# Optimization experiments

Measured on AMD Instinct MI355X. Metric: run time of the kernel, lower is better.

The kernel has to match this reference:

```python
import jax, jax.numpy as jnp
import numpy as np

B, N = 8, 200          # images, padded detections per image
IMG = 640.0            # nominal image size for box coordinates
ALLOWED_CLASSES = (1, 2, 3, 5, 7)  # roi_model.allowed_class_idxs
SCORE_THR = 0.001


def _make_boxes(key, b, n):
    k1, k2, k3, k4 = jax.random.split(key, 4)
    cxy = jax.random.uniform(k1, (b, n, 2), minval=0.0, maxval=IMG)
    wh = jax.random.uniform(k2, (b, n, 2), minval=10.0, maxval=120.0)
    xy1 = cxy - wh / 2.0
    xy2 = cxy + wh / 2.0
    score = jax.random.uniform(k3, (b, n, 1))
    cls = jax.random.randint(k4, (b, n, 1), 0, 10).astype(jnp.float32)
    return jnp.concatenate([xy1, xy2, score, cls], axis=-1)  # [b,n,6]


def setup_inputs() -> dict:
    key = jax.random.key(0)
    k1, k2 = jax.random.split(key)
    return {"boxes1": _make_boxes(k1, B, N), "boxes2": _make_boxes(k2, B, N)}


def _valid(boxes):
    cls = boxes[..., 5].astype(jnp.int32)
    allowed = jnp.zeros(cls.shape, dtype=bool)
    for c in ALLOWED_CLASSES:
        allowed = allowed | (cls == c)
    return (boxes[..., 4] > SCORE_THR) & allowed


def _iou_matrix(b1, b2):
    """Vectorized pairwise IoU; zero where classes differ or a box is filtered out."""
    v1, v2 = _valid(b1), _valid(b2)
    x1 = jnp.maximum(b1[:, :, None, 0], b2[:, None, :, 0])
    y1 = jnp.maximum(b1[:, :, None, 1], b2[:, None, :, 1])
    x2 = jnp.minimum(b1[:, :, None, 2], b2[:, None, :, 2])
    y2 = jnp.minimum(b1[:, :, None, 3], b2[:, None, :, 3])
    inter = jnp.maximum(x2 - x1, 0.0) * jnp.maximum(y2 - y1, 0.0)  # [B,N,N]
    a1 = (b1[..., 2] - b1[..., 0]) * (b1[..., 3] - b1[..., 1])
    a2 = (b2[..., 2] - b2[..., 0]) * (b2[..., 3] - b2[..., 1])
    union = a1[:, :, None] + a2[:, None, :] - inter
    same_cls = b1[..., 5].astype(jnp.int32)[:, :, None] == b2[..., 5].astype(jnp.int32)[:, None, :]
    mask = same_cls & v1[:, :, None] & v2[:, None, :]
    return jnp.where(mask, inter / union, 0.0), v1, v2


def _hungarian(cost):
    """Exact linear sum assignment (minimize) for a square cost matrix.
    Jonker-Volgenant style shortest augmenting path, O(n^3), vectorized inner step.
    Returns col_of_row[i] = column assigned to row i. Padding rows/cols of zeros
    make this equivalent to scipy's rectangular max-IoU matching."""
    n = cost.shape[0]
    INF = np.inf
    a = np.zeros((n + 1, n + 1), dtype=np.float64)
    a[1:, 1:] = cost
    u = np.zeros(n + 1); v = np.zeros(n + 1)
    p = np.zeros(n + 1, dtype=np.int64)   # p[j] = row matched to column j (1-based)
    way = np.zeros(n + 1, dtype=np.int64)
    for i in range(1, n + 1):
        p[0] = i
        j0 = 0
        minv = np.full(n + 1, INF)
        used = np.zeros(n + 1, dtype=bool)
        while True:
            used[j0] = True
            i0 = p[j0]
            cur = a[i0] - u[i0] - v
            cand = (~used) & (cur < minv)
            minv[cand] = cur[cand]
            way[cand] = j0
            masked = np.where(used, INF, minv)
            j0 = int(masked.argmin())
            delta = masked[j0]
            u[p[used]] += delta
            v[used] -= delta
            minv[~used] -= delta
            if p[j0] == 0:
                break
        while j0 != 0:
            j1 = way[j0]
            p[j0] = p[j1]
            j0 = j1
    col_of_row = np.empty(n, dtype=np.int64)
    col_of_row[p[1:] - 1] = np.arange(n)
    return col_of_row


def _loss(iou, perm, na, nb):
    matched = jnp.take_along_axis(iou, perm[:, :, None], axis=2)[..., 0]  # [B,N]
    sum_ious = matched.sum(-1)
    # n_instances = n_pairs + leftovers on each side = max(na, nb)
    denom = jnp.maximum(jnp.maximum(na, nb), 1.0)
    per_img = 1.0 - sum_ious / denom
    both_zero = (na == 0) & (nb == 0)
    one_zero = (na == 0) != (nb == 0)
    per_img = jnp.where(both_zero, 0.0, jnp.where(one_zero, 1.0, per_img))
    return per_img.mean()


def reference(boxes1, boxes2):
    iou, v1, v2 = _iou_matrix(boxes1, boxes2)
    cost = -np.asarray(iou, dtype=np.float64)
    perm = jnp.asarray(np.stack([_hungarian(cost[b]) for b in range(cost.shape[0])]))
    na = v1.sum(-1).astype(jnp.float32)
    nb = v2.sum(-1).astype(jnp.float32)
    return _loss(iou, perm, na, nb)
```

## Files before the change

### kernel.cpp

```cpp
#include <hip/hip_runtime.h>
#include <math.h>


constexpr int BIMG = 8;
constexpr int NBOX = 200;
constexpr int NCLS = 5;
constexpr int NBLK = BIMG * NCLS;
constexpr float SCORE_THR = 0.001f;

__device__ __forceinline__ unsigned fkey(float f) {
    unsigned u = __float_as_uint(f);
    return (u & 0x80000000u) ? ~u : (u | 0x80000000u);
}
__device__ __forceinline__ float fkey_inv(unsigned k) {
    unsigned u = (k & 0x80000000u) ? (k ^ 0x80000000u) : ~k;
    return __uint_as_float(u);
}

#define ARGMIN_DPP_STEP(CTRL)                                                \
    {                                                                        \
        unsigned ok = (unsigned)__builtin_amdgcn_update_dpp(                 \
            (int)ik, (int)ik, (CTRL), 0xF, 0xF, false);                      \
        unsigned op = (unsigned)__builtin_amdgcn_update_dpp(                 \
            (int)ip, (int)ip, (CTRL), 0xF, 0xF, false);                      \
        bool lt = (ok < ik) || ((ok == ik) && (op < ip));                    \
        ik = lt ? ok : ik;                                                   \
        ip = lt ? op : ip;                                                   \
    }

__global__ void __launch_bounds__(64)
det_fused_kernel(const float* __restrict__ boxes1,
                 const float* __restrict__ boxes2,
                 float* __restrict__ sum_part,
                 int* __restrict__ m1_part, int* __restrict__ m2_part,
                 int* __restrict__ flags,
                 float* __restrict__ out)
{
    const int lane = threadIdx.x;
    const int blk  = blockIdx.x;
    const int b    = blk / NCLS;
    const int ci   = blk % NCLS;
    const int cls  = (ci == 0) ? 1 : (ci == 1) ? 2 : (ci == 2) ? 3 : (ci == 3) ? 5 : 7;

    __shared__ float r1x1[NBOX], r1y1[NBOX], r1x2[NBOX], r1y2[NBOX], r1a[NBOX];
    __shared__ float r2x1[NBOX], r2y1[NBOX], r2x2[NBOX], r2y2[NBOX], r2a[NBOX];
    __shared__ float uarr[NBOX + 1], varr[NBOX + 1], minvarr[NBOX + 1];
    __shared__ int   wayarr[NBOX + 1], parr[NBOX + 1], usedarr[NBOX + 1];

    const float* g1 = boxes1 + (size_t)b * NBOX * 6;
    const float* g2 = boxes2 + (size_t)b * NBOX * 6;
    const unsigned long long ltmask = (1ull << lane) - 1ull;

    int m1 = 0, m2 = 0;
    for (int c0 = 0; c0 < NBOX; c0 += 64) {
        int t = c0 + lane;
        bool in = (t < NBOX);
        float x1 = 0, y1 = 0, x2 = 0, y2 = 0, sc = 0, cf = 0;
        if (in) {
            const float2* p = (const float2*)(g1 + (size_t)t * 6);
            float2 q0 = p[0], q1 = p[1], q2 = p[2];
            x1 = q0.x; y1 = q0.y; x2 = q1.x; y2 = q1.y; sc = q2.x; cf = q2.y;
        }
        bool pr = in && (sc > SCORE_THR) && ((int)cf == cls);
        unsigned long long mk = __ballot(pr);
        int pos = m1 + __popcll(mk & ltmask);
        if (pr) { r1x1[pos] = x1; r1y1[pos] = y1; r1x2[pos] = x2; r1y2[pos] = y2;
                  r1a[pos] = (x2 - x1) * (y2 - y1); }
        m1 += __popcll(mk);

        if (in) {
            const float2* p = (const float2*)(g2 + (size_t)t * 6);
            float2 q0 = p[0], q1 = p[1], q2 = p[2];
            x1 = q0.x; y1 = q0.y; x2 = q1.x; y2 = q1.y; sc = q2.x; cf = q2.y;
        }
        pr = in && (sc > SCORE_THR) && ((int)cf == cls);
        mk = __ballot(pr);
        pos = m2 + __popcll(mk & ltmask);
        if (pr) { r2x1[pos] = x1; r2y1[pos] = y1; r2x2[pos] = x2; r2y2[pos] = y2;
                  r2a[pos] = (x2 - x1) * (y2 - y1); }
        m2 += __popcll(mk);
    }
    __syncthreads();

    float blockContrib = 0.f;

    do {
        if (m1 == 0 || m2 == 0) break;
        const int n = (m1 > m2) ? m1 : m2;

        if (n <= 64) {
            const bool swapped = (m1 > m2);
            float* rrx1 = swapped ? r2x1 : r1x1; float* rry1 = swapped ? r2y1 : r1y1;
            float* rrx2 = swapped ? r2x2 : r1x2; float* rry2 = swapped ? r2y2 : r1y2;
            float* rra  = swapped ? r2a  : r1a;
            float* ccx1 = swapped ? r1x1 : r2x1; float* ccy1 = swapped ? r1y1 : r2y1;
            float* ccx2 = swapped ? r1x2 : r2x2; float* ccy2 = swapped ? r1y2 : r2y2;
            float* cca  = swapped ? r1a  : r2a;
            int mr = swapped ? m2 : m1;
            int mc = swapped ? m1 : m2;

            float rbx1 = 0, rby1 = 0, rbx2 = 0, rby2 = 0, rba = 0;
            if (lane < mr) { rbx1 = rrx1[lane]; rby1 = rry1[lane]; rbx2 = rrx2[lane];
                             rby2 = rry2[lane]; rba = rra[lane]; }
            float cbx1 = 0, cby1 = 0, cbx2 = 0, cby2 = 0, cba = 0;
            if (lane < mc) { cbx1 = ccx1[lane]; cby1 = ccy1[lane]; cbx2 = ccx2[lane];
                             cby2 = ccy2[lane]; cba = cca[lane]; }

            unsigned long long rowmask = 0ull;
            bool colnz = false;
            for (int i = 0; i < mr; ++i) {
                float ax1 = rrx1[i], ay1 = rry1[i], ax2 = rrx2[i], ay2 = rry2[i];
                float iw = fminf(ax2, cbx2) - fmaxf(ax1, cbx1);
                float ih = fminf(ay2, cby2) - fmaxf(ay1, cby1);
                bool nz = (lane < mc) && (iw > 0.f) && (ih > 0.f);
                unsigned long long bal = __ballot(nz);
                if (bal) rowmask |= (1ull << i);
                colnz |= nz;
            }
            int mrP = __popcll(rowmask);
            if (mrP == 0) break;
            unsigned long long colmask = __ballot(colnz);
            int mcP = __popcll(colmask);

            __syncthreads();
            if (lane < mr && ((rowmask >> lane) & 1ull)) {
                int pos = __popcll(rowmask & ltmask);
                rrx1[pos] = rbx1; rry1[pos] = rby1; rrx2[pos] = rbx2; rry2[pos] = rby2;
                rra[pos] = rba;
            }
            if (lane < mc && ((colmask >> lane) & 1ull)) {
                int pos = __popcll(colmask & ltmask);
                ccx1[pos] = cbx1; ccy1[pos] = cby1; ccx2[pos] = cbx2; ccy2[pos] = cby2;
                cca[pos] = cba;
            }
            __syncthreads();
            rbx1 = rby1 = rbx2 = rby2 = rba = 0.f;
            if (lane < mrP) { rbx1 = rrx1[lane]; rby1 = rry1[lane]; rbx2 = rrx2[lane];
                              rby2 = rry2[lane]; rba = rra[lane]; }
            cbx1 = cby1 = cbx2 = cby2 = cba = 0.f;
            if (lane < mcP) { cbx1 = ccx1[lane]; cby1 = ccy1[lane]; cbx2 = ccx2[lane];
                              cby2 = ccy2[lane]; cba = cca[lane]; }
            if (mrP > mcP) {
                float t;
                t = rbx1; rbx1 = cbx1; cbx1 = t;  t = rby1; rby1 = cby1; cby1 = t;
                t = rbx2; rbx2 = cbx2; cbx2 = t;  t = rby2; rby2 = cby2; cby2 = t;
                t = rba;  rba  = cba;  cba  = t;
                int ti = mrP; mrP = mcP; mcP = ti;
            }

            float cmin = INFINITY; int cargmin = 0;
            for (int i = 0; i < mrP; ++i) {
                float rx1 = __shfl(rbx1, i), ry1 = __shfl(rby1, i);
                float rx2 = __shfl(rbx2, i), ry2 = __shfl(rby2, i);
                float ra  = __shfl(rba,  i);
                float iw = fmaxf(fminf(rx2, cbx2) - fmaxf(rx1, cbx1), 0.f);
                float ih = fmaxf(fminf(ry2, cby2) - fmaxf(ry1, cby1), 0.f);
                float inter = iw * ih;
                float c = (lane < mcP) ? (-(inter / (ra + cba - inter))) : 0.f;
                if (c < cmin) { cmin = c; cargmin = i; }
            }

            unsigned long long rowfree = (mrP >= 64) ? ~0ull : ((1ull << mrP) - 1ull);
            unsigned long long amask = 0ull;
            for (int j = 0; j < mcP; ++j) {
                int i = __builtin_amdgcn_readlane(cargmin, j);
                if ((rowfree >> i) & 1ull) { rowfree &= ~(1ull << i); amask |= (1ull << j); }
            }

            float vj = (lane < mcP) ? cmin : 0.f;
            float urow = 0.f;
            int   pmrow = 0;
            float cmx1 = 0, cmy1 = 0, cmx2 = 0, cmy2 = 0, cma = 0;
            {
                bool gm = (lane < mcP) && ((amask >> lane) & 1ull);
                float gx1 = __shfl(rbx1, cargmin), gy1 = __shfl(rby1, cargmin);
                float gx2 = __shfl(rbx2, cargmin), gy2 = __shfl(rby2, cargmin);
                float gar = __shfl(rba,  cargmin);
                if (gm) { pmrow = cargmin + 1;
                          cmx1 = gx1; cmy1 = gy1; cmx2 = gx2; cmy2 = gy2; cma = gar; }
            }

            for (int i = 1; i <= mrP; ++i) {
                if (!((rowfree >> (i - 1)) & 1ull)) continue;

                float rootx1 = __shfl(rbx1, i - 1), rooty1 = __shfl(rby1, i - 1);
                float rootx2 = __shfl(rbx2, i - 1), rooty2 = __shfl(rby2, i - 1);
                float roota  = __shfl(rba,  i - 1);
                float rx1 = rootx1, ry1 = rooty1, rx2 = rootx2, ry2 = rooty2, ra = roota;
                float u0 = 0.f, u_free = 0.f, minvj = INFINITY;
                int   wayj = 0, j0cur = 0, j0n = 0;
                bool  usedj = (lane >= mcP);
                bool  found = false;

                for (int guard = 0; guard <= 66; ++guard) {
                    float iou = 0.f;
                    if (lane < mcP) {
                        float iw = fmaxf(fminf(rx2, cbx2) - fmaxf(rx1, cbx1), 0.f);
                        float ih = fmaxf(fminf(ry2, cby2) - fmaxf(ry1, cby1), 0.f);
                        float inter = iw * ih;
                        iou = inter / (ra + cba - inter);
                    }
                    float cur = -iou - u0 - vj;
                    if (!usedj && cur < minvj) { minvj = cur; wayj = j0cur; }

                    unsigned ik = usedj ? 0xFFFFFFFFu : fkey(minvj);
                    unsigned ip = usedj ? 0xFFFFFFFFu
                                        : ((pmrow ? 0x100u : 0u) | (unsigned)(lane + 1));
                    ARGMIN_DPP_STEP(0xB1)
                    ARGMIN_DPP_STEP(0x4E)
                    ARGMIN_DPP_STEP(0x141)
                    ARGMIN_DPP_STEP(0x140)
                    ARGMIN_DPP_STEP(0x142)
                    ARGMIN_DPP_STEP(0x143)
                    unsigned sk = (unsigned)__builtin_amdgcn_readlane((int)ik, 63);
                    unsigned sp = (unsigned)__builtin_amdgcn_readlane((int)ip, 63);
                    float delta = fkey_inv(sk);
                    j0n = (int)(sp & 0xFFu);
                    bool j0matched = (sp & 0x100u) != 0u;
                    if (j0n == 0xFF) break;

                    u_free += delta;
                    if (usedj) { vj -= delta; if (pmrow) urow += delta; }
                    else       { minvj -= delta; }

                    if (!j0matched) { found = true; break; }

                    if (lane == j0n - 1) usedj = true;
                    u0  = __shfl(urow, j0n - 1);
                    rx1 = __shfl(cmx1, j0n - 1); ry1 = __shfl(cmy1, j0n - 1);
                    rx2 = __shfl(cmx2, j0n - 1); ry2 = __shfl(cmy2, j0n - 1);
                    ra  = __shfl(cma,  j0n - 1);
                    j0cur = j0n;
                }

                if (found) {
                    int jj = j0n;
                    for (int hop = 0; hop < 66 && jj != 0; ++hop) {
                        int j1 = __shfl(wayj, jj - 1);
                        if (j1 == 0) {
                            if (lane == jj - 1) {
                                pmrow = i; urow = u_free;
                                cmx1 = rootx1; cmy1 = rooty1; cmx2 = rootx2;
                                cmy2 = rooty2; cma = roota;
                            }
                            jj = 0;
                        } else {
                            int   ppj = __shfl(pmrow, j1 - 1);
                            float pur = __shfl(urow,  j1 - 1);
                            float px1 = __shfl(cmx1, j1 - 1), py1 = __shfl(cmy1, j1 - 1);
                            float px2 = __shfl(cmx2, j1 - 1), py2 = __shfl(cmy2, j1 - 1);
                            float pa  = __shfl(cma,  j1 - 1);
                            if (lane == jj - 1) {
                                pmrow = ppj; urow = pur;
                                cmx1 = px1; cmy1 = py1; cmx2 = px2; cmy2 = py2; cma = pa;
                            }
                            jj = j1;
                        }
                    }
                }
            }

            float contrib = 0.f;
            if (lane < mcP && pmrow != 0) {
                float iw = fmaxf(fminf(cmx2, cbx2) - fmaxf(cmx1, cbx1), 0.f);
                float ih = fmaxf(fminf(cmy2, cby2) - fmaxf(cmy1, cby1), 0.f);
                float inter = iw * ih;
                contrib = inter / (cma + cba - inter);
            }
            #pragma unroll
            for (int off = 32; off; off >>= 1) contrib += __shfl_xor(contrib, off);
            blockContrib = contrib;
        } else {
            for (int j = lane; j <= n; j += 64) { varr[j] = 0.f; parr[j] = 0; uarr[j] = 0.f; }
            __syncthreads();

            int j0 = 0;
            for (int i = 1; i <= n; ++i) {
                if (lane == 0) parr[0] = i;
                for (int j = lane; j <= n; j += 64) { minvarr[j] = INFINITY; usedarr[j] = 0; }
                j0 = 0;
                __syncthreads();

                for (int it = 0; it <= n + 1; ++it) {
                    if (lane == 0) usedarr[j0] = 1;
                    __syncthreads();
                    const int i0 = parr[j0];
                    const float u0 = uarr[i0];
                    const bool rowReal = (i0 <= m1);
                    float rx1 = 0, ry1 = 0, rx2 = 0, ry2 = 0, ra = 0;
                    if (rowReal) { rx1 = r1x1[i0-1]; ry1 = r1y1[i0-1]; rx2 = r1x2[i0-1];
                                   ry2 = r1y2[i0-1]; ra = r1a[i0-1]; }
                    for (int j = lane; j <= n; j += 64) {
                        if (j >= 1 && !usedarr[j]) {
                            float cost = 0.f;
                            if (rowReal && j <= m2) {
                                float ix1 = fmaxf(rx1, r2x1[j-1]), iy1 = fmaxf(ry1, r2y1[j-1]);
                                float ix2 = fminf(rx2, r2x2[j-1]), iy2 = fminf(ry2, r2y2[j-1]);
                                float iw = fmaxf(ix2 - ix1, 0.f), ih = fmaxf(iy2 - iy1, 0.f);
                                float inter = iw * ih;
                                cost = -(inter / (ra + r2a[j-1] - inter));
                            }
                            float cur = cost - u0 - varr[j];
                            if (cur < minvarr[j]) { minvarr[j] = cur; wayarr[j] = j0; }
                        }
                    }
                    __syncthreads();

                    float bv = INFINITY; int bu = 0, bj = n + 1;
                    for (int j = lane; j <= n; j += 64) {
                        float m = usedarr[j] ? INFINITY : minvarr[j];
                        int   un = (parr[j] == 0) ? 1 : 0;
                        if (m < bv || (m == bv && (un > bu || (un == bu && j < bj))))
                            { bv = m; bu = un; bj = j; }
                    }
                    #pragma unroll
                    for (int off = 32; off; off >>= 1) {
                        float ov = __shfl_xor(bv, off);
                        int   ou = __shfl_xor(bu, off);
                        int   oj = __shfl_xor(bj, off);
                        if (ov < bv || (ov == bv && (ou > bu || (ou == bu && oj < bj))))
                            { bv = ov; bu = ou; bj = oj; }
                    }
                    j0 = bj;
                    const float delta = bv;
                    for (int j = lane; j <= n; j += 64) {
                        if (usedarr[j]) { uarr[parr[j]] += delta; varr[j] -= delta; }
                        else            { minvarr[j] -= delta; }
                    }
                    __syncthreads();
                    if (parr[j0] == 0) break;
                }

                if (lane == 0) {
                    int jj = j0, guard = 0;
                    while (jj != 0 && guard++ <= n + 1) {
                        int j1 = wayarr[jj];
                        parr[jj] = parr[j1];
                        jj = j1;
                    }
                }
                __syncthreads();
            }

            float contrib = 0.f;
            for (int j = lane; j <= n; j += 64) {
                if (j >= 1 && j <= m2) {
                    int pi = parr[j];
                    if (pi >= 1 && pi <= m1) {
                        float ix1 = fmaxf(r1x1[pi-1], r2x1[j-1]), iy1 = fmaxf(r1y1[pi-1], r2y1[j-1]);
                        float ix2 = fminf(r1x2[pi-1], r2x2[j-1]), iy2 = fminf(r1y2[pi-1], r2y2[j-1]);
                        float iw = fmaxf(ix2 - ix1, 0.f), ih = fmaxf(iy2 - iy1, 0.f);
                        float inter = iw * ih;
                        contrib += inter / (r1a[pi-1] + r2a[j-1] - inter);
                    }
                }
            }
            #pragma unroll
            for (int off = 32; off; off >>= 1) contrib += __shfl_xor(contrib, off);
            blockContrib = contrib;
        }
    } while (0);

    if (lane == 0) {
        sum_part[blk] = blockContrib;
        m1_part[blk]  = m1;
        m2_part[blk]  = m2;
    }
    if (blk != 0) {
        if (lane == 0)
            __hip_atomic_store(&flags[blk], 1, __ATOMIC_RELEASE, __HIP_MEMORY_SCOPE_AGENT);
        return;
    }

    if (lane >= 1 && lane < NBLK) {
        while (__hip_atomic_load(&flags[lane], __ATOMIC_ACQUIRE,
                                 __HIP_MEMORY_SCOPE_AGENT) != 1)
            __builtin_amdgcn_s_sleep(1);
    }
    float s = 0.f; int a1 = 0, a2 = 0;
    if (lane < NBLK) { s = sum_part[lane]; a1 = m1_part[lane]; a2 = m2_part[lane]; }
    float st = s; int t1 = a1, t2 = a2;
    #pragma unroll
    for (int k = 1; k < NCLS; ++k) {
        st += __shfl(s, lane + k);
        t1 += __shfl(a1, lane + k);
        t2 += __shfl(a2, lane + k);
    }
    float per;
    {
        float denom = fmaxf(fmaxf((float)t1, (float)t2), 1.f);
        float pv = 1.f - st / denom;
        bool bz = (t1 == 0) && (t2 == 0);
        bool oz = ((t1 == 0) != (t2 == 0));
        per = bz ? 0.f : (oz ? 1.f : pv);
    }
    float acc = 0.f;
    #pragma unroll
    for (int bb = 0; bb < BIMG; ++bb) acc += __shfl(per, bb * NCLS);
    if (lane == 0) out[0] = acc / (float)BIMG;
}

extern "C" void kernel_launch(void* const* d_in, const int* in_sizes, int n_in,
                              void* d_out, int out_size, void* d_ws, size_t ws_size,
                              hipStream_t stream) {
    const float* b1 = (const float*)d_in[0];
    const float* b2 = (const float*)d_in[1];
    float* sum_part = (float*)d_ws;
    int*   m1_part  = (int*)(sum_part + NBLK);
    int*   m2_part  = m1_part + NBLK;
    int*   flags    = m2_part + NBLK;

    det_fused_kernel<<<NBLK, 64, 0, stream>>>(b1, b2, sum_part, m1_part, m2_part,
                                              flags, (float*)d_out);
}
```

Baseline: 78.28 us.

## Rewrite wave-level Hungarian with float4 box layout and packed argmin keys

Box storage changes from separate per-coordinate shared arrays to float4 records, with all global loads issued up front into registers. The small-case path fuses the overlap scan with the greedy column-min computation and uses a single packed 32-bit key (truncated value plus matched flag plus lane) for the DPP argmin instead of two keys. Shuffles become readlane, and the final reduction uses DPP. Areas are recomputed instead of stored, and truncating the key's low mantissa bits can change tie-breaking and assignment results.

```diff
diff --git a/kernel.cpp b/kernel.cpp
--- a/kernel.cpp
+++ b/kernel.cpp
@@ -8,24 +8,20 @@
 constexpr int NBLK = BIMG * NCLS;
 constexpr float SCORE_THR = 0.001f;
 
-__device__ __forceinline__ unsigned fkey(float f) {
-    unsigned u = __float_as_uint(f);
-    return (u & 0x80000000u) ? ~u : (u | 0x80000000u);
-}
-__device__ __forceinline__ float fkey_inv(unsigned k) {
-    unsigned u = (k & 0x80000000u) ? (k ^ 0x80000000u) : ~k;
-    return __uint_as_float(u);
-}
-
-#define ARGMIN_DPP_STEP(CTRL)                                                \
+__device__ __forceinline__ int   rl_i(int x, int l)   { return __builtin_amdgcn_readlane(x, l); }
+__device__ __forceinline__ float rl_f(float x, int l) { return __int_as_float(__builtin_amdgcn_readlane(__float_as_int(x), l)); }
+
+#define MIN_DPP_STEP(CTRL)                                                   \
     {                                                                        \
         unsigned ok = (unsigned)__builtin_amdgcn_update_dpp(                 \
-            (int)ik, (int)ik, (CTRL), 0xF, 0xF, false);                      \
-        unsigned op = (unsigned)__builtin_amdgcn_update_dpp(                 \
-            (int)ip, (int)ip, (CTRL), 0xF, 0xF, false);                      \
-        bool lt = (ok < ik) || ((ok == ik) && (op < ip));                    \
-        ik = lt ? ok : ik;                                                   \
-        ip = lt ? op : ip;                                                   \
+            (int)key, (int)key, (CTRL), 0xF, 0xF, false);                    \
+        key = (ok < key) ? ok : key;                                         \
+    }
+#define SUM_DPP_STEP(CTRL)                                                   \
+    {                                                                        \
+        float o = __int_as_float(__builtin_amdgcn_update_dpp(                \
+            __float_as_int(acc), __float_as_int(acc), (CTRL), 0xF, 0xF, false)); \
+        acc += o;                                                            \
     }
 
 __global__ void __launch_bounds__(64)
@@ -41,44 +37,45 @@
     const int b    = blk / NCLS;
     const int ci   = blk % NCLS;
     const int cls  = (ci == 0) ? 1 : (ci == 1) ? 2 : (ci == 2) ? 3 : (ci == 3) ? 5 : 7;
-
-    __shared__ float r1x1[NBOX], r1y1[NBOX], r1x2[NBOX], r1y2[NBOX], r1a[NBOX];
-    __shared__ float r2x1[NBOX], r2y1[NBOX], r2x2[NBOX], r2y2[NBOX], r2a[NBOX];
+    const unsigned long long ltm = (1ull << lane) - 1ull;
+
+    __shared__ float4 bs1[NBOX], bs2[NBOX];
+    __shared__ float4 rcomp[64], ccomp[64];
+    __shared__ float2 cmeta[64];
     __shared__ float uarr[NBOX + 1], varr[NBOX + 1], minvarr[NBOX + 1];
     __shared__ int   wayarr[NBOX + 1], parr[NBOX + 1], usedarr[NBOX + 1];
 
     const float* g1 = boxes1 + (size_t)b * NBOX * 6;
     const float* g2 = boxes2 + (size_t)b * NBOX * 6;
-    const unsigned long long ltmask = (1ull << lane) - 1ull;
-
+
+    float2 A[12], B[12];
+    #pragma unroll
+    for (int c = 0; c < 4; ++c) {
+        int t = c * 64 + lane;
+        if (t < NBOX) {
+            const float2* p = (const float2*)(g1 + (size_t)t * 6);
+            A[3*c] = p[0]; A[3*c+1] = p[1]; A[3*c+2] = p[2];
+            const float2* q = (const float2*)(g2 + (size_t)t * 6);
+            B[3*c] = q[0]; B[3*c+1] = q[1]; B[3*c+2] = q[2];
+        } else {
+            A[3*c] = A[3*c+1] = make_float2(0.f, 0.f); A[3*c+2] = make_float2(0.f, -1.f);
+            B[3*c] = B[3*c+1] = make_float2(0.f, 0.f); B[3*c+2] = make_float2(0.f, -1.f);
+        }
+    }
     int m1 = 0, m2 = 0;
-    for (int c0 = 0; c0 < NBOX; c0 += 64) {
-        int t = c0 + lane;
-        bool in = (t < NBOX);
-        float x1 = 0, y1 = 0, x2 = 0, y2 = 0, sc = 0, cf = 0;
-        if (in) {
-            const float2* p = (const float2*)(g1 + (size_t)t * 6);
-            float2 q0 = p[0], q1 = p[1], q2 = p[2];
-            x1 = q0.x; y1 = q0.y; x2 = q1.x; y2 = q1.y; sc = q2.x; cf = q2.y;
-        }
-        bool pr = in && (sc > SCORE_THR) && ((int)cf == cls);
+    #pragma unroll
+    for (int c = 0; c < 4; ++c) {
+        int t = c * 64 + lane;
+        bool pr = (t < NBOX) && (A[3*c+2].x > SCORE_THR) && ((int)A[3*c+2].y == cls);
         unsigned long long mk = __ballot(pr);
-        int pos = m1 + __popcll(mk & ltmask);
-        if (pr) { r1x1[pos] = x1; r1y1[pos] = y1; r1x2[pos] = x2; r1y2[pos] = y2;
-                  r1a[pos] = (x2 - x1) * (y2 - y1); }
-        m1 += __popcll(mk);
-
-        if (in) {
-            const float2* p = (const float2*)(g2 + (size_t)t * 6);
-            float2 q0 = p[0], q1 = p[1], q2 = p[2];
-            x1 = q0.x; y1 = q0.y; x2 = q1.x; y2 = q1.y; sc = q2.x; cf = q2.y;
-        }
-        pr = in && (sc > SCORE_THR) && ((int)cf == cls);
+        if (pr) bs1[m1 + (int)__popcll(mk & ltm)] =
+            make_float4(A[3*c].x, A[3*c].y, A[3*c+1].x, A[3*c+1].y);
+        m1 += (int)__popcll(mk);
+        pr = (t < NBOX) && (B[3*c+2].x > SCORE_THR) && ((int)B[3*c+2].y == cls);
         mk = __ballot(pr);
-        pos = m2 + __popcll(mk & ltmask);
-        if (pr) { r2x1[pos] = x1; r2y1[pos] = y1; r2x2[pos] = x2; r2y2[pos] = y2;
-                  r2a[pos] = (x2 - x1) * (y2 - y1); }
-        m2 += __popcll(mk);
+        if (pr) bs2[m2 + (int)__popcll(mk & ltm)] =
+            make_float4(B[3*c].x, B[3*c].y, B[3*c+1].x, B[3*c+1].y);
+        m2 += (int)__popcll(mk);
     }
     __syncthreads();
 
@@ -86,240 +83,56 @@
 
     do {
         if (m1 == 0 || m2 == 0) break;
-        const int n = (m1 > m2) ? m1 : m2;
-
-        if (n <= 64) {
-            const bool swapped = (m1 > m2);
-            float* rrx1 = swapped ? r2x1 : r1x1; float* rry1 = swapped ? r2y1 : r1y1;
-            float* rrx2 = swapped ? r2x2 : r1x2; float* rry2 = swapped ? r2y2 : r1y2;
-            float* rra  = swapped ? r2a  : r1a;
-            float* ccx1 = swapped ? r1x1 : r2x1; float* ccy1 = swapped ? r1y1 : r2y1;
-            float* ccx2 = swapped ? r1x2 : r2x2; float* ccy2 = swapped ? r1y2 : r2y2;
-            float* cca  = swapped ? r1a  : r2a;
-            int mr = swapped ? m2 : m1;
-            int mc = swapped ? m1 : m2;
-
-            float rbx1 = 0, rby1 = 0, rbx2 = 0, rby2 = 0, rba = 0;
-            if (lane < mr) { rbx1 = rrx1[lane]; rby1 = rry1[lane]; rbx2 = rrx2[lane];
-                             rby2 = rry2[lane]; rba = rra[lane]; }
-            float cbx1 = 0, cby1 = 0, cbx2 = 0, cby2 = 0, cba = 0;
-            if (lane < mc) { cbx1 = ccx1[lane]; cby1 = ccy1[lane]; cbx2 = ccx2[lane];
-                             cby2 = ccy2[lane]; cba = cca[lane]; }
-
-            unsigned long long rowmask = 0ull;
-            bool colnz = false;
-            for (int i = 0; i < mr; ++i) {
-                float ax1 = rrx1[i], ay1 = rry1[i], ax2 = rrx2[i], ay2 = rry2[i];
-                float iw = fminf(ax2, cbx2) - fmaxf(ax1, cbx1);
-                float ih = fminf(ay2, cby2) - fmaxf(ay1, cby1);
-                bool nz = (lane < mc) && (iw > 0.f) && (ih > 0.f);
-                unsigned long long bal = __ballot(nz);
-                if (bal) rowmask |= (1ull << i);
-                colnz |= nz;
-            }
-            int mrP = __popcll(rowmask);
-            if (mrP == 0) break;
-            unsigned long long colmask = __ballot(colnz);
-            int mcP = __popcll(colmask);
-
-            __syncthreads();
-            if (lane < mr && ((rowmask >> lane) & 1ull)) {
-                int pos = __popcll(rowmask & ltmask);
-                rrx1[pos] = rbx1; rry1[pos] = rby1; rrx2[pos] = rbx2; rry2[pos] = rby2;
-                rra[pos] = rba;
-            }
-            if (lane < mc && ((colmask >> lane) & 1ull)) {
-                int pos = __popcll(colmask & ltmask);
-                ccx1[pos] = cbx1; ccy1[pos] = cby1; ccx2[pos] = cbx2; ccy2[pos] = cby2;
-                cca[pos] = cba;
-            }
-            __syncthreads();
-            rbx1 = rby1 = rbx2 = rby2 = rba = 0.f;
-            if (lane < mrP) { rbx1 = rrx1[lane]; rby1 = rry1[lane]; rbx2 = rrx2[lane];
-                              rby2 = rry2[lane]; rba = rra[lane]; }
-            cbx1 = cby1 = cbx2 = cby2 = cba = 0.f;
-            if (lane < mcP) { cbx1 = ccx1[lane]; cby1 = ccy1[lane]; cbx2 = ccx2[lane];
-                              cby2 = ccy2[lane]; cba = cca[lane]; }
-            if (mrP > mcP) {
-                float t;
-                t = rbx1; rbx1 = cbx1; cbx1 = t;  t = rby1; rby1 = cby1; cby1 = t;
-                t = rbx2; rbx2 = cbx2; cbx2 = t;  t = rby2; rby2 = cby2; cby2 = t;
-                t = rba;  rba  = cba;  cba  = t;
-                int ti = mrP; mrP = mcP; mcP = ti;
-            }
-
-            float cmin = INFINITY; int cargmin = 0;
-            for (int i = 0; i < mrP; ++i) {
-                float rx1 = __shfl(rbx1, i), ry1 = __shfl(rby1, i);
-                float rx2 = __shfl(rbx2, i), ry2 = __shfl(rby2, i);
-                float ra  = __shfl(rba,  i);
-                float iw = fmaxf(fminf(rx2, cbx2) - fmaxf(rx1, cbx1), 0.f);
-                float ih = fmaxf(fminf(ry2, cby2) - fmaxf(ry1, cby1), 0.f);
-                float inter = iw * ih;
-                float c = (lane < mcP) ? (-(inter / (ra + cba - inter))) : 0.f;
-                if (c < cmin) { cmin = c; cargmin = i; }
-            }
-
-            unsigned long long rowfree = (mrP >= 64) ? ~0ull : ((1ull << mrP) - 1ull);
-            unsigned long long amask = 0ull;
-            for (int j = 0; j < mcP; ++j) {
-                int i = __builtin_amdgcn_readlane(cargmin, j);
-                if ((rowfree >> i) & 1ull) { rowfree &= ~(1ull << i); amask |= (1ull << j); }
-            }
-
-            float vj = (lane < mcP) ? cmin : 0.f;
-            float urow = 0.f;
-            int   pmrow = 0;
-            float cmx1 = 0, cmy1 = 0, cmx2 = 0, cmy2 = 0, cma = 0;
-            {
-                bool gm = (lane < mcP) && ((amask >> lane) & 1ull);
-                float gx1 = __shfl(rbx1, cargmin), gy1 = __shfl(rby1, cargmin);
-                float gx2 = __shfl(rbx2, cargmin), gy2 = __shfl(rby2, cargmin);
-                float gar = __shfl(rba,  cargmin);
-                if (gm) { pmrow = cargmin + 1;
-                          cmx1 = gx1; cmy1 = gy1; cmx2 = gx2; cmy2 = gy2; cma = gar; }
-            }
-
-            for (int i = 1; i <= mrP; ++i) {
-                if (!((rowfree >> (i - 1)) & 1ull)) continue;
-
-                float rootx1 = __shfl(rbx1, i - 1), rooty1 = __shfl(rby1, i - 1);
-                float rootx2 = __shfl(rbx2, i - 1), rooty2 = __shfl(rby2, i - 1);
-                float roota  = __shfl(rba,  i - 1);
-                float rx1 = rootx1, ry1 = rooty1, rx2 = rootx2, ry2 = rooty2, ra = roota;
-                float u0 = 0.f, u_free = 0.f, minvj = INFINITY;
-                int   wayj = 0, j0cur = 0, j0n = 0;
-                bool  usedj = (lane >= mcP);
-                bool  found = false;
-
-                for (int guard = 0; guard <= 66; ++guard) {
-                    float iou = 0.f;
-                    if (lane < mcP) {
-                        float iw = fmaxf(fminf(rx2, cbx2) - fmaxf(rx1, cbx1), 0.f);
-                        float ih = fmaxf(fminf(ry2, cby2) - fmaxf(ry1, cby1), 0.f);
-                        float inter = iw * ih;
-                        iou = inter / (ra + cba - inter);
-                    }
-                    float cur = -iou - u0 - vj;
-                    if (!usedj && cur < minvj) { minvj = cur; wayj = j0cur; }
-
-                    unsigned ik = usedj ? 0xFFFFFFFFu : fkey(minvj);
-                    unsigned ip = usedj ? 0xFFFFFFFFu
-                                        : ((pmrow ? 0x100u : 0u) | (unsigned)(lane + 1));
-                    ARGMIN_DPP_STEP(0xB1)
-                    ARGMIN_DPP_STEP(0x4E)
-                    ARGMIN_DPP_STEP(0x141)
-                    ARGMIN_DPP_STEP(0x140)
-                    ARGMIN_DPP_STEP(0x142)
-                    ARGMIN_DPP_STEP(0x143)
-                    unsigned sk = (unsigned)__builtin_amdgcn_readlane((int)ik, 63);
-                    unsigned sp = (unsigned)__builtin_amdgcn_readlane((int)ip, 63);
-                    float delta = fkey_inv(sk);
-                    j0n = (int)(sp & 0xFFu);
-                    bool j0matched = (sp & 0x100u) != 0u;
-                    if (j0n == 0xFF) break;
-
-                    u_free += delta;
-                    if (usedj) { vj -= delta; if (pmrow) urow += delta; }
-                    else       { minvj -= delta; }
-
-                    if (!j0matched) { found = true; break; }
-
-                    if (lane == j0n - 1) usedj = true;
-                    u0  = __shfl(urow, j0n - 1);
-                    rx1 = __shfl(cmx1, j0n - 1); ry1 = __shfl(cmy1, j0n - 1);
-                    rx2 = __shfl(cmx2, j0n - 1); ry2 = __shfl(cmy2, j0n - 1);
-                    ra  = __shfl(cma,  j0n - 1);
-                    j0cur = j0n;
-                }
-
-                if (found) {
-                    int jj = j0n;
-                    for (int hop = 0; hop < 66 && jj != 0; ++hop) {
-                        int j1 = __shfl(wayj, jj - 1);
-                        if (j1 == 0) {
-                            if (lane == jj - 1) {
-                                pmrow = i; urow = u_free;
-                                cmx1 = rootx1; cmy1 = rooty1; cmx2 = rootx2;
-                                cmy2 = rooty2; cma = roota;
-                            }
-                            jj = 0;
-                        } else {
-                            int   ppj = __shfl(pmrow, j1 - 1);
-                            float pur = __shfl(urow,  j1 - 1);
-                            float px1 = __shfl(cmx1, j1 - 1), py1 = __shfl(cmy1, j1 - 1);
-                            float px2 = __shfl(cmx2, j1 - 1), py2 = __shfl(cmy2, j1 - 1);
-                            float pa  = __shfl(cma,  j1 - 1);
-                            if (lane == jj - 1) {
-                                pmrow = ppj; urow = pur;
-                                cmx1 = px1; cmy1 = py1; cmx2 = px2; cmy2 = py2; cma = pa;
-                            }
-                            jj = j1;
-                        }
-                    }
-                }
-            }
-
-            float contrib = 0.f;
-            if (lane < mcP && pmrow != 0) {
-                float iw = fmaxf(fminf(cmx2, cbx2) - fmaxf(cmx1, cbx1), 0.f);
-                float ih = fmaxf(fminf(cmy2, cby2) - fmaxf(cmy1, cby1), 0.f);
-                float inter = iw * ih;
-                contrib = inter / (cma + cba - inter);
-            }
-            #pragma unroll
-            for (int off = 32; off; off >>= 1) contrib += __shfl_xor(contrib, off);
-            blockContrib = contrib;
-        } else {
+        const int nmax = (m1 > m2) ? m1 : m2;
+
+        if (nmax > 64) {
+            const int n = nmax;
             for (int j = lane; j <= n; j += 64) { varr[j] = 0.f; parr[j] = 0; uarr[j] = 0.f; }
             __syncthreads();
-
             int j0 = 0;
-            for (int i = 1; i <= n; ++i) {
-                if (lane == 0) parr[0] = i;
+            for (int i2 = 1; i2 <= n; ++i2) {
+                if (lane == 0) parr[0] = i2;
                 for (int j = lane; j <= n; j += 64) { minvarr[j] = INFINITY; usedarr[j] = 0; }
                 j0 = 0;
                 __syncthreads();
-
                 for (int it = 0; it <= n + 1; ++it) {
                     if (lane == 0) usedarr[j0] = 1;
                     __syncthreads();
                     const int i0 = parr[j0];
                     const float u0 = uarr[i0];
                     const bool rowReal = (i0 <= m1);
-                    float rx1 = 0, ry1 = 0, rx2 = 0, ry2 = 0, ra = 0;
-                    if (rowReal) { rx1 = r1x1[i0-1]; ry1 = r1y1[i0-1]; rx2 = r1x2[i0-1];
-                                   ry2 = r1y2[i0-1]; ra = r1a[i0-1]; }
+                    float4 rbx = make_float4(0,0,0,0); float ra = 0.f;
+                    if (rowReal) { rbx = bs1[i0-1]; ra = (rbx.z-rbx.x)*(rbx.w-rbx.y); }
                     for (int j = lane; j <= n; j += 64) {
                         if (j >= 1 && !usedarr[j]) {
                             float cost = 0.f;
                             if (rowReal && j <= m2) {
-                                float ix1 = fmaxf(rx1, r2x1[j-1]), iy1 = fmaxf(ry1, r2y1[j-1]);
-                                float ix2 = fminf(rx2, r2x2[j-1]), iy2 = fminf(ry2, r2y2[j-1]);
-                                float iw = fmaxf(ix2 - ix1, 0.f), ih = fmaxf(iy2 - iy1, 0.f);
+                                float4 cbx = bs2[j-1];
+                                float iw = fmaxf(fminf(rbx.z, cbx.z) - fmaxf(rbx.x, cbx.x), 0.f);
+                                float ih = fmaxf(fminf(rbx.w, cbx.w) - fmaxf(rbx.y, cbx.y), 0.f);
                                 float inter = iw * ih;
-                                cost = -(inter / (ra + r2a[j-1] - inter));
+                                float ca = (cbx.z-cbx.x)*(cbx.w-cbx.y);
+                                cost = -(inter / (ra + ca - inter));
                             }
-                            float cur = cost - u0 - varr[j];
-                            if (cur < minvarr[j]) { minvarr[j] = cur; wayarr[j] = j0; }
+                            float curv = cost - u0 - varr[j];
+                            if (curv < minvarr[j]) { minvarr[j] = curv; wayarr[j] = j0; }
                         }
                     }
                     __syncthreads();
-
                     float bv = INFINITY; int bu = 0, bj = n + 1;
                     for (int j = lane; j <= n; j += 64) {
                         float m = usedarr[j] ? INFINITY : minvarr[j];
-                        int   un = (parr[j] == 0) ? 1 : 0;
+                        int un = (parr[j] == 0) ? 1 : 0;
                         if (m < bv || (m == bv && (un > bu || (un == bu && j < bj))))
                             { bv = m; bu = un; bj = j; }
                     }
                     #pragma unroll
                     for (int off = 32; off; off >>= 1) {
-                        float ov = __shfl_xor(bv, off);
-                        int   ou = __shfl_xor(bu, off);
-                        int   oj = __shfl_xor(bj, off);
-                        if (ov < bv || (ov == bv && (ou > bu || (ou == bu && oj < bj))))
-                            { bv = ov; bu = ou; bj = oj; }
+                        float ov2 = __shfl_xor(bv, off);
+                        int ou = __shfl_xor(bu, off);
+                        int oj = __shfl_xor(bj, off);
+                        if (ov2 < bv || (ov2 == bv && (ou > bu || (ou == bu && oj < bj))))
+                            { bv = ov2; bu = ou; bj = oj; }
                     }
                     j0 = bj;
                     const float delta = bv;
@@ -330,35 +143,192 @@
                     __syncthreads();
                     if (parr[j0] == 0) break;
                 }
-
                 if (lane == 0) {
-                    int jj = j0, guard = 0;
-                    while (jj != 0 && guard++ <= n + 1) {
-                        int j1 = wayarr[jj];
-                        parr[jj] = parr[j1];
-                        jj = j1;
-                    }
+                    int jj = j0, gg = 0;
+                    while (jj != 0 && gg++ <= n + 1) { int j1 = wayarr[jj]; parr[jj] = parr[j1]; jj = j1; }
                 }
                 __syncthreads();
             }
-
             float contrib = 0.f;
             for (int j = lane; j <= n; j += 64) {
                 if (j >= 1 && j <= m2) {
                     int pi = parr[j];
                     if (pi >= 1 && pi <= m1) {
-                        float ix1 = fmaxf(r1x1[pi-1], r2x1[j-1]), iy1 = fmaxf(r1y1[pi-1], r2y1[j-1]);
-                        float ix2 = fminf(r1x2[pi-1], r2x2[j-1]), iy2 = fminf(r1y2[pi-1], r2y2[j-1]);
-                        float iw = fmaxf(ix2 - ix1, 0.f), ih = fmaxf(iy2 - iy1, 0.f);
+                        float4 rbx = bs1[pi-1], cbx = bs2[j-1];
+                        float iw = fmaxf(fminf(rbx.z, cbx.z) - fmaxf(rbx.x, cbx.x), 0.f);
+                        float ih = fmaxf(fminf(rbx.w, cbx.w) - fmaxf(rbx.y, cbx.y), 0.f);
                         float inter = iw * ih;
-                        contrib += inter / (r1a[pi-1] + r2a[j-1] - inter);
+                        float ra = (rbx.z-rbx.x)*(rbx.w-rbx.y);
+                        float ca = (cbx.z-cbx.x)*(cbx.w-cbx.y);
+                        contrib += inter / (ra + ca - inter);
                     }
                 }
             }
             #pragma unroll
             for (int off = 32; off; off >>= 1) contrib += __shfl_xor(contrib, off);
             blockContrib = contrib;
-        }
+            break;
+        }
+
+        const bool sw = (m1 > m2);
+        const float4* rS = sw ? bs2 : bs1;
+        const float4* cS = sw ? bs1 : bs2;
+        const int mr = sw ? m2 : m1;
+        const int mc = sw ? m1 : m2;
+
+        float4 cb = make_float4(0,0,0,0);
+        if (lane < mc) cb = cS[lane];
+        float cba = (cb.z - cb.x) * (cb.w - cb.y);
+
+        unsigned long long rowmask = 0ull;
+        float cmin = 0.f; int carg = -1;
+        #define SCAN1(ii)                                                      \
+        {                                                                      \
+            float4 rbv = rS[(ii)];                                             \
+            float iw = fminf(rbv.z, cb.z) - fmaxf(rbv.x, cb.x);                \
+            float ih = fminf(rbv.w, cb.w) - fmaxf(rbv.y, cb.y);                \
+            bool ov = (lane < mc) && (iw > 0.f) && (ih > 0.f);                 \
+            unsigned long long bal = __ballot(ov);                             \
+            if (bal) rowmask |= (1ull << (ii));                                \
+            if (ov) {                                                          \
+                float inter = iw * ih;                                         \
+                float ra2 = (rbv.z - rbv.x) * (rbv.w - rbv.y);                 \
+                float cst = -(inter / (ra2 + cba - inter));                    \
+                if (cst < cmin) { cmin = cst; carg = (ii); }                   \
+            }                                                                  \
+        }
+        int i = 0;
+        for (; i + 4 <= mr; i += 4) { SCAN1(i) SCAN1(i+1) SCAN1(i+2) SCAN1(i+3) }
+        for (; i < mr; ++i) { SCAN1(i) }
+        #undef SCAN1
+
+        const int mrP = (int)__popcll(rowmask);
+        if (mrP == 0) break;
+        const unsigned long long colmask = __ballot(carg >= 0);
+        const int mcP = (int)__popcll(colmask);
+        const int nC = (mrP > mcP) ? mrP : mcP;
+
+        int cargc = (carg >= 0) ? (int)__popcll(rowmask & ((1ull << carg) - 1ull)) : 0;
+
+        if (lane < mr && ((rowmask >> lane) & 1ull))
+            rcomp[(int)__popcll(rowmask & ltm)] = rS[lane];
+        if (lane < mc && carg >= 0) {
+            int cp = (int)__popcll(colmask & ltm);
+            ccomp[cp] = cb;
+            cmeta[cp] = make_float2(cmin, __int_as_float(cargc));
+        }
+        __syncthreads();
+        float4 rb = make_float4(0,0,0,0);
+        if (lane < mrP) rb = rcomp[lane];
+        cb = make_float4(0,0,0,0); cba = 0.f;
+        float vj = 0.f; int cargf = 0;
+        if (lane < mcP) {
+            cb = ccomp[lane];
+            cba = (cb.z - cb.x) * (cb.w - cb.y);
+            float2 cm2 = cmeta[lane];
+            vj = cm2.x; cargf = __float_as_int(cm2.y);
+        }
+
+        unsigned long long rowfree = (mrP >= 64) ? ~0ull : ((1ull << mrP) - 1ull);
+        unsigned long long amask = 0ull;
+        for (int j = 0; j < mcP; ++j) {
+            int ia = rl_i(cargf, j);
+            if ((rowfree >> ia) & 1ull) { rowfree &= ~(1ull << ia); amask |= (1ull << j); }
+        }
+        int   pmrow = 0;
+        float urow  = 0.f;
+        float4 cm = make_float4(0,0,0,0);
+        {
+            float gx = __shfl(rb.x, cargf), gy = __shfl(rb.y, cargf);
+            float gz = __shfl(rb.z, cargf), gw = __shfl(rb.w, cargf);
+            bool gm = (lane < mcP) && ((amask >> lane) & 1ull);
+            if (gm) { pmrow = cargf + 1; cm = make_float4(gx, gy, gz, gw); }
+        }
+
+        for (int r = 1; r <= mrP; ++r) {
+            if (!((rowfree >> (r - 1)) & 1ull)) continue;
+
+            const float rtx = rl_f(rb.x, r-1), rty = rl_f(rb.y, r-1);
+            const float rtz = rl_f(rb.z, r-1), rtw = rl_f(rb.w, r-1);
+            float rx = rtx, ry = rty, rz = rtz, rw = rtw;
+            float ra = (rz - rx) * (rw - ry);
+            float u0 = 0.f, u_free = 0.f, minvj = INFINITY;
+            int   wayj = 0, j0cur = 0, j0n = 0;
+            bool  usedj = (lane >= nC);
+            bool  found = false;
+
+            for (int guard = 0; guard <= 66; ++guard) {
+                float iou = 0.f;
+                if (lane < mcP) {
+                    float iw = fmaxf(fminf(rz, cb.z) - fmaxf(rx, cb.x), 0.f);
+                    float ih = fmaxf(fminf(rw, cb.w) - fmaxf(ry, cb.y), 0.f);
+                    float inter = iw * ih;
+                    iou = inter / (ra + cba - inter);
+                }
+                float cur = -iou - u0 - vj;
+                if (!usedj && cur < minvj) { minvj = cur; wayj = j0cur; }
+
+                unsigned key = 0xFFFFFFFFu;
+                if (!usedj)
+                    key = ((__float_as_uint(minvj) | 0x80000000u) & 0xFFFFFF80u)
+                          | (pmrow ? 64u : 0u) | (unsigned)lane;
+                MIN_DPP_STEP(0xB1)  MIN_DPP_STEP(0x4E)  MIN_DPP_STEP(0x141)
+                MIN_DPP_STEP(0x140) MIN_DPP_STEP(0x142) MIN_DPP_STEP(0x143)
+                unsigned k63 = (unsigned)rl_i((int)key, 63);
+                if (k63 == 0xFFFFFFFFu) break;
+                const int   jl    = (int)(k63 & 63u);
+                const float delta = rl_f(minvj, jl);
+
+                u_free += delta;
+                if (usedj) { vj -= delta; urow += delta; }
+                else       { minvj -= delta; }
+
+                if (!(k63 & 64u)) { j0n = jl + 1; found = true; break; }
+
+                if (lane == jl) usedj = true;
+                u0 = rl_f(urow, jl);
+                rx = rl_f(cm.x, jl); ry = rl_f(cm.y, jl);
+                rz = rl_f(cm.z, jl); rw = rl_f(cm.w, jl);
+                ra = (rz - rx) * (rw - ry);
+                j0cur = jl + 1;
+            }
+
+            if (!found) continue;
+
+            {
+                int src = (wayj > 0) ? (wayj - 1) : 0;
+                int   pp = __shfl(pmrow, src);
+                float pu = __shfl(urow,  src);
+                float p0 = __shfl(cm.x, src), p1 = __shfl(cm.y, src);
+                float p2 = __shfl(cm.z, src), p3 = __shfl(cm.w, src);
+                bool fromRoot = (wayj == 0);
+                int   np = fromRoot ? r      : pp;
+                float nu = fromRoot ? u_free : pu;
+                float n0 = fromRoot ? rtx : p0, n1 = fromRoot ? rty : p1;
+                float n2 = fromRoot ? rtz : p2, n3 = fromRoot ? rtw : p3;
+                int jj = j0n;
+                for (int hop = 0; hop < 66 && jj != 0; ++hop) {
+                    int j1 = rl_i(wayj, jj - 1);
+                    if (lane == jj - 1) {
+                        pmrow = np; urow = nu;
+                        cm = make_float4(n0, n1, n2, n3);
+                    }
+                    jj = j1;
+                }
+            }
+        }
+
+        float acc = 0.f;
+        if (lane < mcP && pmrow != 0) {
+            float iw = fmaxf(fminf(cm.z, cb.z) - fmaxf(cm.x, cb.x), 0.f);
+            float ih = fmaxf(fminf(cm.w, cb.w) - fmaxf(cm.y, cb.y), 0.f);
+            float inter = iw * ih;
+            float cmA = (cm.z - cm.x) * (cm.w - cm.y);
+            acc = inter / (cmA + cba - inter);
+        }
+        SUM_DPP_STEP(0xB1)  SUM_DPP_STEP(0x4E)  SUM_DPP_STEP(0x141)
+        SUM_DPP_STEP(0x140) SUM_DPP_STEP(0x142) SUM_DPP_STEP(0x143)
+        blockContrib = rl_f(acc, 63);
     } while (0);
 
     if (lane == 0) {
@@ -394,10 +364,10 @@
         bool oz = ((t1 == 0) != (t2 == 0));
         per = bz ? 0.f : (oz ? 1.f : pv);
     }
-    float acc = 0.f;
+    float accm = 0.f;
     #pragma unroll
-    for (int bb = 0; bb < BIMG; ++bb) acc += __shfl(per, bb * NCLS);
-    if (lane == 0) out[0] = acc / (float)BIMG;
+    for (int bb = 0; bb < BIMG; ++bb) accm += __shfl(per, bb * NCLS);
+    if (lane == 0) out[0] = accm / (float)BIMG;
 }
 
 extern "C" void kernel_launch(void* const* d_in, const int* in_sizes, int n_in,
```

New measurement: 83.02 us. 1.06x slower.
